# Performance work log

Hardware: AMD Instinct MI355X
Metric: run time of the kernel (lower is better)

Reference implementation:

```python
import jax, jax.numpy as jnp
import numpy as np

N = 100000          # nodes
E = 1_600_000       # edges (nnz of sparse adj)
IN_F = 256
OUT_F = 128
DROP_P = 0.2


def setup_inputs() -> dict:
    key = jax.random.key(0)
    k1, k2, k3, k4, k5, k6 = jax.random.split(key, 6)
    return {
        "input": jax.random.normal(k1, (N, IN_F), dtype=jnp.float32),
        "weight": jax.random.normal(k2, (IN_F, OUT_F), dtype=jnp.float32) * 0.05,
        "adj_row": jax.random.randint(k3, (E,), 0, N, dtype=jnp.int32),
        "adj_col": jax.random.randint(k4, (E,), 0, N, dtype=jnp.int32),
        "adj_val": jax.random.uniform(k5, (E,), dtype=jnp.float32),
        "drop_u": jax.random.uniform(k6, (N, IN_F), dtype=jnp.float32),
    }


def reference(input, weight, adj_row, adj_col, adj_val, drop_u):
    # F.dropout(input, p, training=True): zero with prob p, scale survivors by 1/(1-p)
    x = jnp.where(drop_u > DROP_P, input / (1.0 - DROP_P), 0.0)
    # dense projection: [N, in] @ [in, out] -> [N, out]
    support = x @ weight
    # SpMM: out[r] = sum over edges e with row==r of val[e] * support[col[e]]
    gathered = support[adj_col] * adj_val[:, None]          # [E, out]
    output = jax.ops.segment_sum(gathered, adj_row, num_segments=N)  # [N, out]
    return output
```

## Files before the change

### kernel.cpp

```cpp
#include <hip/hip_runtime.h>

#define N_NODES 100000
#define IN_F 256
#define OUT_F 128
#define NB 782
#define CAP 2560
#define QCAP 896
#define TILE 4096

typedef __attribute__((ext_vector_type(8))) short v8s;
typedef __attribute__((ext_vector_type(4))) float v4f;

__device__ __forceinline__ unsigned short f2bf(float f) {
    unsigned int u = __float_as_uint(f);
    u += 0x7fffu + ((u >> 16) & 1u);
    return (unsigned short)(u >> 16);
}
__device__ __forceinline__ float bf2f(unsigned short s) {
    return __uint_as_float((unsigned int)s << 16);
}

__global__ void wt_kernel(const float* __restrict__ w, unsigned short* __restrict__ bt) {
    int idx = blockIdx.x * 256 + threadIdx.x;
    int k = idx >> 7;
    int n = idx & 127;
    bt[n * IN_F + k] = f2bf(w[idx]);
}

__global__ __launch_bounds__(256) void gemm_kernel(
    const float* __restrict__ x, const float* __restrict__ u,
    const unsigned short* __restrict__ bt, unsigned short* __restrict__ support) {
    __shared__ unsigned short As[128 * 72];
    __shared__ unsigned short Bs[128 * 72];

    const int tid  = threadIdx.x;
    const int lane = tid & 63;
    const int wv   = tid >> 6;
    const int wr   = wv >> 1, wc = wv & 1;
    const long long base = (long long)blockIdx.x * 128;

    v4f acc[4][4] = {};

    for (int k0 = 0; k0 < IN_F; k0 += 64) {
        if (k0) __syncthreads();
        {
            const int row = tid >> 1;
            const int kh  = (tid & 1) * 32;
            long long g = base + row;
            unsigned short* dst = &As[row * 72 + kh];
            if (g < N_NODES) {
                const float* xs = x + g * IN_F + k0 + kh;
                const float* us = u + g * IN_F + k0 + kh;
                #pragma unroll
                for (int i = 0; i < 8; ++i) {
                    float4 xi = *(const float4*)(xs + i * 4);
                    float4 du = *(const float4*)(us + i * 4);
                    ushort4 pk;
                    pk.x = f2bf(du.x > 0.2f ? xi.x * 1.25f : 0.0f);
                    pk.y = f2bf(du.y > 0.2f ? xi.y * 1.25f : 0.0f);
                    pk.z = f2bf(du.z > 0.2f ? xi.z * 1.25f : 0.0f);
                    pk.w = f2bf(du.w > 0.2f ? xi.w * 1.25f : 0.0f);
                    *(ushort4*)(dst + i * 4) = pk;
                }
            } else {
                #pragma unroll
                for (int i = 0; i < 4; ++i)
                    *(v8s*)(dst + i * 8) = (v8s){0,0,0,0,0,0,0,0};
            }
        }
        {
            const int n  = tid >> 1;
            const int kh = (tid & 1) * 32;
            const unsigned short* src = bt + n * IN_F + k0 + kh;
            unsigned short* dst = &Bs[n * 72 + kh];
            #pragma unroll
            for (int i = 0; i < 4; ++i)
                *(v8s*)(dst + i * 8) = *(const v8s*)(src + i * 8);
        }
        __syncthreads();
        #pragma unroll
        for (int ks = 0; ks < 2; ++ks) {
            const int kb = ks * 32 + (lane >> 4) * 8;
            v8s af[4], bf[4];
            #pragma unroll
            for (int t = 0; t < 4; ++t)
                af[t] = *(const v8s*)&As[(wr * 64 + t * 16 + (lane & 15)) * 72 + kb];
            #pragma unroll
            for (int t = 0; t < 4; ++t)
                bf[t] = *(const v8s*)&Bs[(wc * 64 + t * 16 + (lane & 15)) * 72 + kb];
            #pragma unroll
            for (int tm = 0; tm < 4; ++tm)
                #pragma unroll
                for (int tn = 0; tn < 4; ++tn)
                    acc[tm][tn] = __builtin_amdgcn_mfma_f32_16x16x32_bf16(
                        af[tm], bf[tn], acc[tm][tn], 0, 0, 0);
        }
    }
    const int rq = lane >> 4;
    const int cl = lane & 15;
    #pragma unroll
    for (int tm = 0; tm < 4; ++tm) {
        #pragma unroll
        for (int r = 0; r < 4; ++r) {
            long long g = base + wr * 64 + tm * 16 + rq * 4 + r;
            if (g < N_NODES) {
                unsigned short* o = support + g * OUT_F + wc * 64 + cl;
                #pragma unroll
                for (int tn = 0; tn < 4; ++tn)
                    o[tn * 16] = f2bf(acc[tm][tn][r]);
            }
        }
    }
}

__global__ void init_kernel(int* __restrict__ cursor) {
    int i = blockIdx.x * 256 + threadIdx.x;
    if (i < NB) cursor[i * 16] = i * CAP;
}

__global__ __launch_bounds__(256) void scatter_kernel(
    const int* __restrict__ row, const int* __restrict__ col,
    const float* __restrict__ val, int* __restrict__ cursor,
    int2* __restrict__ cv, int E) {
    __shared__ int cnt[1024];
    __shared__ int loc[1024];
    __shared__ int delta[1024];
    __shared__ int tmp[256];
    __shared__ int gd[TILE];
    __shared__ int2 stage[TILE];
    __shared__ int total_s;
    const int tid = threadIdx.x;
    const int base_e = blockIdx.x * TILE;

    for (int i = tid; i < 1024; i += 256) cnt[i] = 0;
    __syncthreads();
    #pragma unroll
    for (int j = 0; j < TILE / 256; ++j) {
        int e = base_e + j * 256 + tid;
        if (e < E) atomicAdd(&cnt[row[e] >> 7], 1);
    }
    __syncthreads();
    int c0 = cnt[4*tid], c1 = cnt[4*tid+1], c2 = cnt[4*tid+2], c3 = cnt[4*tid+3];
    int s = c0 + c1 + c2 + c3;
    tmp[tid] = s;
    __syncthreads();
    #pragma unroll
    for (int d = 1; d < 256; d <<= 1) {
        int t = (tid >= d) ? tmp[tid - d] : 0;
        __syncthreads();
        tmp[tid] += t;
        __syncthreads();
    }
    int excl = tmp[tid] - s;
    loc[4*tid]   = excl;
    loc[4*tid+1] = excl + c0;
    loc[4*tid+2] = excl + c0 + c1;
    loc[4*tid+3] = excl + c0 + c1 + c2;
    if (tid == 255) total_s = tmp[255];
    __syncthreads();
    for (int i = tid; i < NB; i += 256) {
        int c = cnt[i];
        int gbase = 0;
        if (c > 0) gbase = atomicAdd(&cursor[i * 16], c);
        delta[i] = gbase - loc[i];
        cnt[i] = loc[i];
    }
    __syncthreads();
    #pragma unroll
    for (int j = 0; j < TILE / 256; ++j) {
        int e = base_e + j * 256 + tid;
        if (e < E) {
            int r = row[e];
            int b = r >> 7;
            int rank = atomicAdd(&cnt[b], 1);
            stage[rank] = make_int2(col[e] | ((r & 127) << 17), __float_as_int(val[e]));
            gd[rank] = delta[b] + rank;
        }
    }
    __syncthreads();
    int total = total_s;
    for (int i = tid; i < total; i += 256)
        cv[gd[i]] = stage[i];
}

__global__ __launch_bounds__(256) void acc2_kernel(
    const int* __restrict__ cursor, const int2* __restrict__ cv,
    const unsigned short* __restrict__ support, float* __restrict__ out) {
    __shared__ int2 sorted[QCAP];
    __shared__ int cnt_s[32];
    __shared__ int start_s[32];
    __shared__ int pos_s[32];
    const int tid = threadIdx.x;
    const int bq = blockIdx.x;
    const int b = bq >> 2;
    const int q = bq & 3;
    const int e0 = b * CAP;
    const int nE = cursor[b * 16] - e0;

    if (tid < 32) cnt_s[tid] = 0;
    __syncthreads();
    for (int i = tid; i < nE; i += 256) {
        int cx = cv[e0 + i].x;
        int lr = cx >> 17;
        if ((lr >> 5) == q) atomicAdd(&cnt_s[lr & 31], 1);
    }
    __syncthreads();
    if (tid < 32) {
        int v = cnt_s[tid];
        int sc = v;
        #pragma unroll
        for (int d = 1; d < 32; d <<= 1) {
            int t = __shfl_up(sc, d, 64);
            if (tid >= d) sc += t;
        }
        start_s[tid] = sc - v;
        pos_s[tid] = sc - v;
    }
    __syncthreads();
    for (int i = tid; i < nE; i += 256) {
        int2 c = cv[e0 + i];
        int lr = c.x >> 17;
        if ((lr >> 5) == q) {
            int rank = atomicAdd(&pos_s[lr & 31], 1);
            sorted[rank] = c;
        }
    }
    __syncthreads();
    const int lane = tid & 63, w = tid >> 6;
    const long long rowbase = (long long)b * 128 + q * 32;
    for (int rr = 0; rr < 8; ++rr) {
        int rl = w * 8 + rr;
        int e = start_s[rl];
        int end = e + cnt_s[rl];
        float a0 = 0.f, a1 = 0.f;
        for (; e < end; e += 4) {
            #pragma unroll
            for (int j = 0; j < 4; ++j) {
                int idx = e + j;
                int ids = min(idx, end - 1);
                int2 c = sorted[ids];
                float vv = (idx < end) ? __int_as_float(c.y) : 0.0f;
                int colv = c.x & 131071;
                unsigned int uu = *(const unsigned int*)(support + colv * OUT_F + lane * 2);
                a0 = fmaf(vv, bf2f((unsigned short)(uu & 0xffff)), a0);
                a1 = fmaf(vv, bf2f((unsigned short)(uu >> 16)), a1);
            }
        }
        long long g = rowbase + rl;
        if (g < N_NODES)
            *(float2*)(out + g * OUT_F + lane * 2) = make_float2(a0, a1);
    }
}

extern "C" void kernel_launch(void* const* d_in, const int* in_sizes, int n_in,
                              void* d_out, int out_size, void* d_ws, size_t ws_size,
                              hipStream_t stream) {
    const float* input   = (const float*)d_in[0];
    const float* weight  = (const float*)d_in[1];
    const int*   adj_row = (const int*)d_in[2];
    const int*   adj_col = (const int*)d_in[3];
    const float* adj_val = (const float*)d_in[4];
    const float* drop_u  = (const float*)d_in[5];
    float* out = (float*)d_out;
    const int E = in_sizes[2];

    char* p = (char*)d_ws;
    unsigned short* bt      = (unsigned short*)p;  p += 65536;
    int2*           cv      = (int2*)p;            p += (size_t)NB * CAP * sizeof(int2);
    unsigned short* support = (unsigned short*)p;  p += (size_t)N_NODES * OUT_F * 2;
    int*            cursor  = (int*)p;

    init_kernel<<<4, 256, 0, stream>>>(cursor);
    wt_kernel<<<128, 256, 0, stream>>>(weight, bt);
    gemm_kernel<<<(N_NODES + 127) / 128, 256, 0, stream>>>(input, drop_u, bt, support);
    scatter_kernel<<<(E + TILE - 1) / TILE, 256, 0, stream>>>(adj_row, adj_col, adj_val, cursor, cv, E);
    acc2_kernel<<<NB * 4, 256, 0, stream>>>(cursor, cv, support, out);
}
```

Measured before the change: 393.5 us.

## Stream A operand directly into registers in GEMM and cache bucket edges in registers

The GEMM now builds the dropout-masked bf16 A fragments straight from global memory into registers, skipping the LDS staging of A. It uses 64-row blocks with one 16-row strip per wave and a double-buffered B tile in LDS, so the weight load overlaps compute. The SpMM bucket kernel reads each edge from global memory once into a fixed register array of 10 per thread, rather than reading the bucket twice for count and placement. In exchange the GEMM gets no A reuse across waves, issues narrower loads, and syncs more often, and the register cache assumes every bucket holds at most CAP edges.

```diff
diff --git a/kernel.cpp b/kernel.cpp
--- a/kernel.cpp
+++ b/kernel.cpp
@@ -7,6 +7,7 @@
 #define CAP 2560
 #define QCAP 896
 #define TILE 4096
+#define BPAD 42
 
 typedef __attribute__((ext_vector_type(8))) short v8s;
 typedef __attribute__((ext_vector_type(4))) float v4f;
@@ -30,85 +31,75 @@
 __global__ __launch_bounds__(256) void gemm_kernel(
     const float* __restrict__ x, const float* __restrict__ u,
     const unsigned short* __restrict__ bt, unsigned short* __restrict__ support) {
-    __shared__ unsigned short As[128 * 72];
-    __shared__ unsigned short Bs[128 * 72];
+    __shared__ unsigned short Bs[2][128 * BPAD];
 
     const int tid  = threadIdx.x;
     const int lane = tid & 63;
     const int wv   = tid >> 6;
-    const int wr   = wv >> 1, wc = wv & 1;
-    const long long base = (long long)blockIdx.x * 128;
-
-    v4f acc[4][4] = {};
-
-    for (int k0 = 0; k0 < IN_F; k0 += 64) {
-        if (k0) __syncthreads();
-        {
-            const int row = tid >> 1;
-            const int kh  = (tid & 1) * 32;
-            long long g = base + row;
-            unsigned short* dst = &As[row * 72 + kh];
-            if (g < N_NODES) {
-                const float* xs = x + g * IN_F + k0 + kh;
-                const float* us = u + g * IN_F + k0 + kh;
-                #pragma unroll
-                for (int i = 0; i < 8; ++i) {
-                    float4 xi = *(const float4*)(xs + i * 4);
-                    float4 du = *(const float4*)(us + i * 4);
-                    ushort4 pk;
-                    pk.x = f2bf(du.x > 0.2f ? xi.x * 1.25f : 0.0f);
-                    pk.y = f2bf(du.y > 0.2f ? xi.y * 1.25f : 0.0f);
-                    pk.z = f2bf(du.z > 0.2f ? xi.z * 1.25f : 0.0f);
-                    pk.w = f2bf(du.w > 0.2f ? xi.w * 1.25f : 0.0f);
-                    *(ushort4*)(dst + i * 4) = pk;
-                }
-            } else {
-                #pragma unroll
-                for (int i = 0; i < 4; ++i)
-                    *(v8s*)(dst + i * 8) = (v8s){0,0,0,0,0,0,0,0};
-            }
-        }
-        {
-            const int n  = tid >> 1;
-            const int kh = (tid & 1) * 32;
-            const unsigned short* src = bt + n * IN_F + k0 + kh;
-            unsigned short* dst = &Bs[n * 72 + kh];
+    const int cl   = lane & 15;
+    const int kq   = lane >> 4;
+    const long long row = (long long)blockIdx.x * 64 + wv * 16 + cl;
+    const bool rv = row < N_NODES;
+    const long long rowc = rv ? row : (N_NODES - 1);
+    const float* xs = x + rowc * IN_F + kq * 8;
+    const float* us = u + rowc * IN_F + kq * 8;
+    const float m = rv ? 1.25f : 0.0f;
+
+    const int scol = tid >> 1;
+    const int skh  = (tid & 1) * 16;
+    const unsigned short* bsrc = bt + scol * IN_F + skh;
+    unsigned short* bdst0 = &Bs[0][scol * BPAD + skh];
+    unsigned short* bdst1 = &Bs[1][scol * BPAD + skh];
+
+    v4f acc[8] = {};
+
+    *(v8s*)(bdst0)     = *(const v8s*)(bsrc);
+    *(v8s*)(bdst0 + 8) = *(const v8s*)(bsrc + 8);
+    __syncthreads();
+
+    #pragma unroll
+    for (int s = 0; s < 8; ++s) {
+        const int k0 = s * 32;
+        float4 x0 = *(const float4*)(xs + k0);
+        float4 x1 = *(const float4*)(xs + k0 + 4);
+        float4 u0 = *(const float4*)(us + k0);
+        float4 u1 = *(const float4*)(us + k0 + 4);
+        if (s < 7) {
+            const unsigned short* src = bsrc + (s + 1) * 32;
+            unsigned short* dst = (s & 1) ? bdst0 : bdst1;
+            *(v8s*)(dst)     = *(const v8s*)(src);
+            *(v8s*)(dst + 8) = *(const v8s*)(src + 8);
+        }
+        const unsigned short* bb = (s & 1) ? &Bs[1][0] : &Bs[0][0];
+        v8s bf[8];
+        #pragma unroll
+        for (int tn = 0; tn < 8; ++tn)
+            bf[tn] = *(const v8s*)&bb[(tn * 16 + cl) * BPAD + kq * 8];
+        unsigned short t0 = f2bf(u0.x > 0.2f ? x0.x * m : 0.0f);
+        unsigned short t1 = f2bf(u0.y > 0.2f ? x0.y * m : 0.0f);
+        unsigned short t2 = f2bf(u0.z > 0.2f ? x0.z * m : 0.0f);
+        unsigned short t3 = f2bf(u0.w > 0.2f ? x0.w * m : 0.0f);
+        unsigned short t4 = f2bf(u1.x > 0.2f ? x1.x * m : 0.0f);
+        unsigned short t5 = f2bf(u1.y > 0.2f ? x1.y * m : 0.0f);
+        unsigned short t6 = f2bf(u1.z > 0.2f ? x1.z * m : 0.0f);
+        unsigned short t7 = f2bf(u1.w > 0.2f ? x1.w * m : 0.0f);
+        v8s af = {(short)t0, (short)t1, (short)t2, (short)t3,
+                  (short)t4, (short)t5, (short)t6, (short)t7};
+        #pragma unroll
+        for (int tn = 0; tn < 8; ++tn)
+            acc[tn] = __builtin_amdgcn_mfma_f32_16x16x32_bf16(af, bf[tn], acc[tn], 0, 0, 0);
+        __syncthreads();
+    }
+
+    const int rq = lane >> 4;
+    #pragma unroll
+    for (int r = 0; r < 4; ++r) {
+        long long g = (long long)blockIdx.x * 64 + wv * 16 + rq * 4 + r;
+        if (g < N_NODES) {
+            unsigned short* o = support + g * OUT_F + cl;
             #pragma unroll
-            for (int i = 0; i < 4; ++i)
-                *(v8s*)(dst + i * 8) = *(const v8s*)(src + i * 8);
-        }
-        __syncthreads();
-        #pragma unroll
-        for (int ks = 0; ks < 2; ++ks) {
-            const int kb = ks * 32 + (lane >> 4) * 8;
-            v8s af[4], bf[4];
-            #pragma unroll
-            for (int t = 0; t < 4; ++t)
-                af[t] = *(const v8s*)&As[(wr * 64 + t * 16 + (lane & 15)) * 72 + kb];
-            #pragma unroll
-            for (int t = 0; t < 4; ++t)
-                bf[t] = *(const v8s*)&Bs[(wc * 64 + t * 16 + (lane & 15)) * 72 + kb];
-            #pragma unroll
-            for (int tm = 0; tm < 4; ++tm)
-                #pragma unroll
-                for (int tn = 0; tn < 4; ++tn)
-                    acc[tm][tn] = __builtin_amdgcn_mfma_f32_16x16x32_bf16(
-                        af[tm], bf[tn], acc[tm][tn], 0, 0, 0);
-        }
-    }
-    const int rq = lane >> 4;
-    const int cl = lane & 15;
-    #pragma unroll
-    for (int tm = 0; tm < 4; ++tm) {
-        #pragma unroll
-        for (int r = 0; r < 4; ++r) {
-            long long g = base + wr * 64 + tm * 16 + rq * 4 + r;
-            if (g < N_NODES) {
-                unsigned short* o = support + g * OUT_F + wc * 64 + cl;
-                #pragma unroll
-                for (int tn = 0; tn < 4; ++tn)
-                    o[tn * 16] = f2bf(acc[tm][tn][r]);
-            }
+            for (int tn = 0; tn < 8; ++tn)
+                o[tn * 16] = f2bf(acc[tn][r]);
         }
     }
 }
@@ -199,10 +190,17 @@
 
     if (tid < 32) cnt_s[tid] = 0;
     __syncthreads();
-    for (int i = tid; i < nE; i += 256) {
-        int cx = cv[e0 + i].x;
-        int lr = cx >> 17;
-        if ((lr >> 5) == q) atomicAdd(&cnt_s[lr & 31], 1);
+    int2 ej[10];
+    int  vj[10];
+    #pragma unroll
+    for (int j = 0; j < 10; ++j) {
+        int i = j * 256 + tid;
+        int2 c = cv[e0 + i];
+        int lr = (c.x >> 17) & 127;
+        int mine = (i < nE) && ((lr >> 5) == q);
+        ej[j] = c;
+        vj[j] = mine ? (lr & 31) : -1;
+        if (mine) atomicAdd(&cnt_s[lr & 31], 1);
     }
     __syncthreads();
     if (tid < 32) {
@@ -217,12 +215,11 @@
         pos_s[tid] = sc - v;
     }
     __syncthreads();
-    for (int i = tid; i < nE; i += 256) {
-        int2 c = cv[e0 + i];
-        int lr = c.x >> 17;
-        if ((lr >> 5) == q) {
-            int rank = atomicAdd(&pos_s[lr & 31], 1);
-            sorted[rank] = c;
+    #pragma unroll
+    for (int j = 0; j < 10; ++j) {
+        if (vj[j] >= 0) {
+            int rank = atomicAdd(&pos_s[vj[j]], 1);
+            sorted[rank] = ej[j];
         }
     }
     __syncthreads();
@@ -272,7 +269,7 @@
 
     init_kernel<<<4, 256, 0, stream>>>(cursor);
     wt_kernel<<<128, 256, 0, stream>>>(weight, bt);
-    gemm_kernel<<<(N_NODES + 127) / 128, 256, 0, stream>>>(input, drop_u, bt, support);
+    gemm_kernel<<<(N_NODES + 63) / 64, 256, 0, stream>>>(input, drop_u, bt, support);
     scatter_kernel<<<(E + TILE - 1) / TILE, 256, 0, stream>>>(adj_row, adj_col, adj_val, cursor, cv, E);
     acc2_kernel<<<NB * 4, 256, 0, stream>>>(cursor, cv, support, out);
 }
```

New measurement: 384.2 us. 1.02x faster.
